# Kernel tuning notes

Hardware: AMD Instinct MI355X
Metric: run time of the kernel (lower is better)

Reference implementation:

```python
import jax, jax.numpy as jnp
import numpy as np
import math

B, N, T, F_IN, F_OUT = 4, 512, 128, 64, 64


def setup_inputs() -> dict:
    key = jax.random.key(0)
    k1, k2, k3 = jax.random.split(key, 3)
    x = jax.random.normal(k1, (B, N, T, F_IN), dtype=jnp.float32)
    adj = jax.random.uniform(k2, (N, N), dtype=jnp.float32)
    theta_w = jax.random.normal(k3, (F_OUT, F_IN), dtype=jnp.float32) * (1.0 / math.sqrt(F_IN))
    return {"x": x, "sym_norm_Adj_matrix": adj, "Theta_w": theta_w}


def reference(x, sym_norm_Adj_matrix, Theta_w):
    b, n, t, f_in = x.shape
    inv_sqrt_f = 1.0 / math.sqrt(f_in)
    # (B, N, T, F) -> (B*T, N, F)
    xt = jnp.transpose(x, (0, 2, 1, 3)).reshape(b * t, n, f_in)
    # attention scores per (batch*time): (BT, N, N)
    score = jnp.einsum('gnf,gmf->gnm', xt, xt) * inv_sqrt_f
    score = jax.nn.softmax(score, axis=-1) * inv_sqrt_f  # second /sqrt(F_in) in forward
    # post-softmax multiplicative adjacency masking, then graph conv matmul
    masked = sym_norm_Adj_matrix[None, :, :] * score      # (BT, N, N)
    agg = jnp.einsum('gnm,gmf->gnf', masked, xt)          # (BT, N, F_in)
    out = jax.nn.relu(agg @ Theta_w.T)                    # (BT, N, F_out)
    # (B, T, N, F_out) -> (B, N, T, F_out)
    return jnp.transpose(out.reshape(b, t, n, -1), (0, 2, 1, 3))
```

## Files before the change

kernel.cpp:

```cpp
#include <hip/hip_runtime.h>
#include <math.h>

#define B_   4
#define N_   512
#define T_   128
#define F_   64
#define QT   128
#define NSTR (T_*F_)
#define RSR  144
#define RSC  136

typedef __attribute__((ext_vector_type(8))) short  s8v;
typedef __attribute__((ext_vector_type(4))) float  f4v;

union F8 { s8v v; unsigned u[4]; uint2 u2[2]; };

__device__ __forceinline__ int swzR(int row, int col ) {
    return row*RSR + ((((col>>3) ^ (row>>3)) & 7) << 4) + ((col & 7) << 1);
}

__device__ __forceinline__ unsigned cvt_pk(float lo, float hi) {
    unsigned r;
    asm("v_cvt_pk_bf16_f32 %0, %1, %2" : "=v"(r) : "v"(lo), "v"(hi));
    return r;
}

__global__ __launch_bounds__(256, 2)
void sgcn_mfma2_kernel(const float* __restrict__ x,
                       const float* __restrict__ adj,
                       const float* __restrict__ theta,
                       float* __restrict__ out)
{
    __shared__ char ldsbuf[64*RSR + 64*RSC];
    char* Xrow = ldsbuf;
    char* Xcol = ldsbuf + 64*RSR;

    const int tid  = threadIdx.x;
    const int lane = tid & 63;
    const int w    = tid >> 6;
    const int c15  = lane & 15;
    const int g4   = lane >> 4;

    const int g  = blockIdx.y;
    const int b  = g >> 7;
    const int t  = g & 127;
    const int q0 = blockIdx.x*QT + 32*w;

    const float* xg = x + (size_t)b*N_*NSTR + (size_t)t*F_;

    F8 qf[2][2];
    #pragma unroll
    for (int qt = 0; qt < 2; ++qt)
      #pragma unroll
      for (int kk = 0; kk < 2; ++kk) {
        const float* qp = xg + (size_t)(q0 + 16*qt + c15)*NSTR + 32*kk + 8*g4;
        float4 a = *(const float4*)qp;
        float4 c = *(const float4*)(qp + 4);
        qf[qt][kk].u[0] = cvt_pk(a.x, a.y);
        qf[qt][kk].u[1] = cvt_pk(a.z, a.w);
        qf[qt][kk].u[2] = cvt_pk(c.x, c.y);
        qf[qt][kk].u[3] = cvt_pk(c.z, c.w);
      }

    f4v  Oacc[4][2];
    float l_acc[2] = {0.f, 0.f};
    #pragma unroll
    for (int ft = 0; ft < 4; ++ft)
      #pragma unroll
      for (int qt = 0; qt < 2; ++qt) Oacc[ft][qt] = (f4v)0.f;

    const int nrow = tid >> 4;
    const int nb   = 4*w;

    float4 xv[4];
    #pragma unroll
    for (int it = 0; it < 4; ++it)
        xv[it] = *(const float4*)(xg + (size_t)(nrow + 16*it)*NSTR + 4*c15);

    for (int kt = 0; kt < 8; ++kt) {
        __syncthreads();

        #pragma unroll
        for (int it = 0; it < 4; ++it) {
            int n = nrow + 16*it;
            unsigned p0 = cvt_pk(xv[it].x, xv[it].y);
            unsigned p1 = cvt_pk(xv[it].z, xv[it].w);
            *(uint2*)(Xrow + swzR(n, 4*c15)) = make_uint2(p0, p1);

            unsigned t0 = (unsigned)__shfl_xor((int)p0, 16);
            unsigned t1 = (unsigned)__shfl_xor((int)p1, 16);
            unsigned a  = (g4 & 2) ? p1 : p0;
            unsigned ta = (g4 & 2) ? t1 : t0;
            unsigned bq = (g4 & 2) ? p0 : p1;
            unsigned tb = (g4 & 2) ? t0 : t1;
            unsigned u_mine = (g4 & 1) ? ((ta >> 16) | (a  & 0xffff0000u))
                                       : ((a  & 0xffffu) | (ta << 16));
            unsigned u_oth  = (g4 & 1) ? ((tb >> 16) | (bq & 0xffff0000u))
                                       : ((bq & 0xffffu) | (tb << 16));
            unsigned v2 = (unsigned)__shfl_xor((int)u_oth, 32);
            uint2 wv = (g4 & 2) ? make_uint2(v2, u_mine) : make_uint2(u_mine, v2);
            *(uint2*)(Xcol + (4*c15 + g4)*RSC + (nb + 16*it)*2) = wv;
        }

        __syncthreads();

        if (kt < 7) {
            #pragma unroll
            for (int it = 0; it < 4; ++it)
                xv[it] = *(const float4*)(xg + (size_t)((kt+1)*64 + nrow + 16*it)*NSTR + 4*c15);
        }

        float4 adjv[2][4];
        #pragma unroll
        for (int qt = 0; qt < 2; ++qt)
          #pragma unroll
          for (int mt = 0; mt < 4; ++mt)
            adjv[qt][mt] = *(const float4*)(adj + (size_t)(q0 + 16*qt + c15)*N_ + kt*64 + 16*mt + 4*g4);

        f4v S[4][2];
        #pragma unroll
        for (int mt = 0; mt < 4; ++mt)
          #pragma unroll
          for (int qt = 0; qt < 2; ++qt) S[mt][qt] = (f4v)0.f;

        #pragma unroll
        for (int kk = 0; kk < 2; ++kk)
          #pragma unroll
          for (int mt = 0; mt < 4; ++mt) {
            F8 af;
            af.v = *(const s8v*)(Xrow + swzR(16*mt + c15, 32*kk + 8*g4));
            #pragma unroll
            for (int qt = 0; qt < 2; ++qt)
              S[mt][qt] = __builtin_amdgcn_mfma_f32_16x16x32_bf16(af.v, qf[qt][kk].v, S[mt][qt], 0, 0, 0);
          }

        F8 pb[2][2];
        #pragma unroll
        for (int qt = 0; qt < 2; ++qt)
          #pragma unroll
          for (int mt = 0; mt < 4; ++mt) {
            float e0 = __expf(S[mt][qt][0] * 0.125f);
            float e1 = __expf(S[mt][qt][1] * 0.125f);
            float e2 = __expf(S[mt][qt][2] * 0.125f);
            float e3 = __expf(S[mt][qt][3] * 0.125f);
            l_acc[qt] += (e0 + e1) + (e2 + e3);
            float4 av = adjv[qt][mt];
            pb[qt][mt>>1].u[2*(mt&1)  ] = cvt_pk(e0*av.x, e1*av.y);
            pb[qt][mt>>1].u[2*(mt&1)+1] = cvt_pk(e2*av.z, e3*av.w);
          }

        #pragma unroll
        for (int kk = 0; kk < 2; ++kk)
          #pragma unroll
          for (int ft = 0; ft < 4; ++ft) {
            F8 vf;
            vf.u2[0] = *(const uint2*)(Xcol + (16*ft + c15)*RSC + 64*kk + 8*g4);
            vf.u2[1] = *(const uint2*)(Xcol + (16*ft + c15)*RSC + 64*kk + 32 + 8*g4);
            #pragma unroll
            for (int qt = 0; qt < 2; ++qt)
              Oacc[ft][qt] = __builtin_amdgcn_mfma_f32_16x16x32_bf16(vf.v, pb[qt][kk].v, Oacc[ft][qt], 0, 0, 0);
          }
    }

    float inv[2];
    #pragma unroll
    for (int qt = 0; qt < 2; ++qt) {
        float lv = l_acc[qt];
        lv += __shfl_xor(lv, 16);
        lv += __shfl_xor(lv, 32);
        inv[qt] = 0.125f / lv;
    }

    F8 ob[2][2];
    #pragma unroll
    for (int qt = 0; qt < 2; ++qt)
      #pragma unroll
      for (int kk = 0; kk < 2; ++kk) {
        f4v o0 = Oacc[2*kk][qt], o1 = Oacc[2*kk+1][qt];
        ob[qt][kk].u[0] = cvt_pk(o0[0]*inv[qt], o0[1]*inv[qt]);
        ob[qt][kk].u[1] = cvt_pk(o0[2]*inv[qt], o0[3]*inv[qt]);
        ob[qt][kk].u[2] = cvt_pk(o1[0]*inv[qt], o1[1]*inv[qt]);
        ob[qt][kk].u[3] = cvt_pk(o1[2]*inv[qt], o1[3]*inv[qt]);
      }

    F8 tf[4][2];
    #pragma unroll
    for (int ot = 0; ot < 4; ++ot)
      #pragma unroll
      for (int kk = 0; kk < 2; ++kk) {
        const float* tp = theta + (size_t)(16*ot + c15)*F_ + 32*kk + 4*g4;
        float4 a = *(const float4*)tp;
        float4 c = *(const float4*)(tp + 16);
        tf[ot][kk].u[0] = cvt_pk(a.x, a.y);
        tf[ot][kk].u[1] = cvt_pk(a.z, a.w);
        tf[ot][kk].u[2] = cvt_pk(c.x, c.y);
        tf[ot][kk].u[3] = cvt_pk(c.z, c.w);
      }

    f4v R[4][2];
    #pragma unroll
    for (int ot = 0; ot < 4; ++ot)
      #pragma unroll
      for (int qt = 0; qt < 2; ++qt) R[ot][qt] = (f4v)0.f;

    #pragma unroll
    for (int kk = 0; kk < 2; ++kk)
      #pragma unroll
      for (int ot = 0; ot < 4; ++ot)
        #pragma unroll
        for (int qt = 0; qt < 2; ++qt)
          R[ot][qt] = __builtin_amdgcn_mfma_f32_16x16x32_bf16(tf[ot][kk].v, ob[qt][kk].v, R[ot][qt], 0, 0, 0);

    #pragma unroll
    for (int ot = 0; ot < 4; ++ot)
      #pragma unroll
      for (int qt = 0; qt < 2; ++qt) {
        float4 v;
        v.x = fmaxf(R[ot][qt][0], 0.f);
        v.y = fmaxf(R[ot][qt][1], 0.f);
        v.z = fmaxf(R[ot][qt][2], 0.f);
        v.w = fmaxf(R[ot][qt][3], 0.f);
        int q  = q0 + 16*qt + c15;
        int fo = 16*ot + 4*g4;
        *(float4*)(out + ((size_t)(b*N_ + q)*T_ + t)*F_ + fo) = v;
      }
}

extern "C" void kernel_launch(void* const* d_in, const int* in_sizes, int n_in,
                              void* d_out, int out_size, void* d_ws, size_t ws_size,
                              hipStream_t stream) {
    const float* x     = (const float*)d_in[0];
    const float* adj   = (const float*)d_in[1];
    const float* theta = (const float*)d_in[2];
    float* out = (float*)d_out;

    dim3 grid(N_ / QT, B_ * T_);
    sgcn_mfma2_kernel<<<grid, 256, 0, stream>>>(x, adj, theta, out);
}
```

Baseline: 106.6 us.

## Double-buffer LDS tiles, swizzle column buffer, use exp2, raise occupancy hint

Splits the X row/column LDS tiles into two buffers so the next key tile is converted and staged during the current tile's softmax and PV MFMAs, cutting one barrier per iteration. The transposed column buffer now uses the same XOR swizzle as the row buffer to reduce bank conflicts. The exponential becomes a native exp2 with the log2e factor folded into the scale, and launch bounds ask for 4 blocks per CU. The cost is twice the LDS per block and tighter register limits, which could cause spills.

Result: slower. 261.6 us (+145.5%).

```diff
diff --git a/kernel.cpp b/kernel.cpp
--- a/kernel.cpp
+++ b/kernel.cpp
@@ -7,16 +7,15 @@
 #define F_   64
 #define QT   128
 #define NSTR (T_*F_)
-#define RSR  144
-#define RSC  136
+#define RS   144
 
 typedef __attribute__((ext_vector_type(8))) short  s8v;
 typedef __attribute__((ext_vector_type(4))) float  f4v;
 
 union F8 { s8v v; unsigned u[4]; uint2 u2[2]; };
 
-__device__ __forceinline__ int swzR(int row, int col ) {
-    return row*RSR + ((((col>>3) ^ (row>>3)) & 7) << 4) + ((col & 7) << 1);
+__device__ __forceinline__ int swz(int row, int col) {
+    return row*RS + ((((col>>3) ^ (row>>3)) & 7) << 4) + ((col & 7) << 1);
 }
 
 __device__ __forceinline__ unsigned cvt_pk(float lo, float hi) {
@@ -25,15 +24,15 @@
     return r;
 }
 
-__global__ __launch_bounds__(256, 2)
-void sgcn_mfma2_kernel(const float* __restrict__ x,
+#define EXPK 0.18033688f
+
+__global__ __launch_bounds__(256, 4)
+void sgcn_mfma4_kernel(const float* __restrict__ x,
                        const float* __restrict__ adj,
                        const float* __restrict__ theta,
                        float* __restrict__ out)
 {
-    __shared__ char ldsbuf[64*RSR + 64*RSC];
-    char* Xrow = ldsbuf;
-    char* Xcol = ldsbuf + 64*RSR;
+    __shared__ char ldsbuf[4*64*RS];
 
     const int tid  = threadIdx.x;
     const int lane = tid & 63;
@@ -72,20 +71,13 @@
     const int nrow = tid >> 4;
     const int nb   = 4*w;
 
-    float4 xv[4];
-    #pragma unroll
-    for (int it = 0; it < 4; ++it)
-        xv[it] = *(const float4*)(xg + (size_t)(nrow + 16*it)*NSTR + 4*c15);
-
-    for (int kt = 0; kt < 8; ++kt) {
-        __syncthreads();
-
+    auto stage = [&](char* Xr, char* Xc, const float4* xvv) {
         #pragma unroll
         for (int it = 0; it < 4; ++it) {
             int n = nrow + 16*it;
-            unsigned p0 = cvt_pk(xv[it].x, xv[it].y);
-            unsigned p1 = cvt_pk(xv[it].z, xv[it].w);
-            *(uint2*)(Xrow + swzR(n, 4*c15)) = make_uint2(p0, p1);
+            unsigned p0 = cvt_pk(xvv[it].x, xvv[it].y);
+            unsigned p1 = cvt_pk(xvv[it].z, xvv[it].w);
+            *(uint2*)(Xr + swz(n, 4*c15)) = make_uint2(p0, p1);
 
             unsigned t0 = (unsigned)__shfl_xor((int)p0, 16);
             unsigned t1 = (unsigned)__shfl_xor((int)p1, 16);
@@ -99,10 +91,23 @@
                                        : ((bq & 0xffffu) | (tb << 16));
             unsigned v2 = (unsigned)__shfl_xor((int)u_oth, 32);
             uint2 wv = (g4 & 2) ? make_uint2(v2, u_mine) : make_uint2(u_mine, v2);
-            *(uint2*)(Xcol + (4*c15 + g4)*RSC + (nb + 16*it)*2) = wv;
+            *(uint2*)(Xc + swz(4*c15 + g4, nb + 16*it)) = wv;
         }
-
+    };
+
+    float4 xv[4];
+    #pragma unroll
+    for (int it = 0; it < 4; ++it)
+        xv[it] = *(const float4*)(xg + (size_t)(nrow + 16*it)*NSTR + 4*c15);
+    stage(ldsbuf, ldsbuf + 64*RS, xv);
+
+    for (int kt = 0; kt < 8; ++kt) {
         __syncthreads();
+
+        char* XrowC = ldsbuf + (size_t)(kt & 1) * (2*64*RS);
+        char* XcolC = XrowC + 64*RS;
+        char* XrowN = ldsbuf + (size_t)((kt & 1) ^ 1) * (2*64*RS);
+        char* XcolN = XrowN + 64*RS;
 
         if (kt < 7) {
             #pragma unroll
@@ -128,7 +133,7 @@
           #pragma unroll
           for (int mt = 0; mt < 4; ++mt) {
             F8 af;
-            af.v = *(const s8v*)(Xrow + swzR(16*mt + c15, 32*kk + 8*g4));
+            af.v = *(const s8v*)(XrowC + swz(16*mt + c15, 32*kk + 8*g4));
             #pragma unroll
             for (int qt = 0; qt < 2; ++qt)
               S[mt][qt] = __builtin_amdgcn_mfma_f32_16x16x32_bf16(af.v, qf[qt][kk].v, S[mt][qt], 0, 0, 0);
@@ -139,23 +144,25 @@
         for (int qt = 0; qt < 2; ++qt)
           #pragma unroll
           for (int mt = 0; mt < 4; ++mt) {
-            float e0 = __expf(S[mt][qt][0] * 0.125f);
-            float e1 = __expf(S[mt][qt][1] * 0.125f);
-            float e2 = __expf(S[mt][qt][2] * 0.125f);
-            float e3 = __expf(S[mt][qt][3] * 0.125f);
+            float e0 = __builtin_amdgcn_exp2f(S[mt][qt][0] * EXPK);
+            float e1 = __builtin_amdgcn_exp2f(S[mt][qt][1] * EXPK);
+            float e2 = __builtin_amdgcn_exp2f(S[mt][qt][2] * EXPK);
+            float e3 = __builtin_amdgcn_exp2f(S[mt][qt][3] * EXPK);
             l_acc[qt] += (e0 + e1) + (e2 + e3);
             float4 av = adjv[qt][mt];
             pb[qt][mt>>1].u[2*(mt&1)  ] = cvt_pk(e0*av.x, e1*av.y);
             pb[qt][mt>>1].u[2*(mt&1)+1] = cvt_pk(e2*av.z, e3*av.w);
           }
 
+        if (kt < 7) stage(XrowN, XcolN, xv);
+
         #pragma unroll
         for (int kk = 0; kk < 2; ++kk)
           #pragma unroll
           for (int ft = 0; ft < 4; ++ft) {
             F8 vf;
-            vf.u2[0] = *(const uint2*)(Xcol + (16*ft + c15)*RSC + 64*kk + 8*g4);
-            vf.u2[1] = *(const uint2*)(Xcol + (16*ft + c15)*RSC + 64*kk + 32 + 8*g4);
+            vf.u2[0] = *(const uint2*)(XcolC + swz(16*ft + c15, 32*kk + 4*g4));
+            vf.u2[1] = *(const uint2*)(XcolC + swz(16*ft + c15, 32*kk + 16 + 4*g4));
             #pragma unroll
             for (int qt = 0; qt < 2; ++qt)
               Oacc[ft][qt] = __builtin_amdgcn_mfma_f32_16x16x32_bf16(vf.v, pb[qt][kk].v, Oacc[ft][qt], 0, 0, 0);
@@ -235,5 +242,5 @@
     float* out = (float*)d_out;
 
     dim3 grid(N_ / QT, B_ * T_);
-    sgcn_mfma2_kernel<<<grid, 256, 0, stream>>>(x, adj, theta, out);
-}
+    sgcn_mfma4_kernel<<<grid, 256, 0, stream>>>(x, adj, theta, out);
+}
```
